# Performance work log

Measured on AMD Instinct MI355X. Metric: run time of the kernel, lower is better.

Reference implementation:

```python
import jax, jax.numpy as jnp
import numpy as np

B, S, D, H = 2, 2048, 1024, 16
HD = D // H  # 64

def setup_inputs() -> dict:
    key = jax.random.key(0)
    ks = jax.random.split(key, 6)
    s = 1.0 / np.sqrt(D)
    return {
        "x": jax.random.normal(ks[0], (B, S, D), dtype=jnp.float32),
        "wq": jax.random.normal(ks[1], (D, D), dtype=jnp.float32) * s,
        "wk": jax.random.normal(ks[2], (D, D), dtype=jnp.float32) * s,
        "wv": jax.random.normal(ks[3], (D, D), dtype=jnp.float32) * s,
        "wo": jax.random.normal(ks[4], (D, D), dtype=jnp.float32) * s,
        "bo": jax.random.normal(ks[5], (D,), dtype=jnp.float32) * 0.01,
    }

def reference(x, wq, wk, wv, wo, bo):
    b, s, _ = x.shape
    # QKV projections (qkvBias=False), reshape to [b, h, s, hd]
    q = (x @ wq).reshape(b, s, H, HD).transpose(0, 2, 1, 3)
    k = (x @ wk).reshape(b, s, H, HD).transpose(0, 2, 1, 3)
    v = (x @ wv).reshape(b, s, H, HD).transpose(0, 2, 1, 3)
    # scores, causal mask (upper triangle -> -inf), scale, softmax
    scores = jnp.einsum('bhqd,bhkd->bhqk', q, k)
    causal = jnp.triu(jnp.ones((s, s), dtype=bool), k=1)
    scores = jnp.where(causal, -jnp.inf, scores) / np.sqrt(HD)
    weights = jax.nn.softmax(scores, axis=-1)  # dropout=0 (eval)
    ctx = jnp.einsum('bhqk,bhkd->bhqd', weights, v)
    ctx = ctx.transpose(0, 2, 1, 3).reshape(b, s, D)
    return ctx @ wo + bo
```

## Files before the change

kernel.cpp:

```cpp
#include <hip/hip_runtime.h>
#include <hip/hip_bf16.h>
#include <math.h>

#define BB 2
#define SS 2048
#define DD 1024
#define HH 16
#define HDIM 64

typedef unsigned short u16;
typedef __attribute__((ext_vector_type(8))) short bfrag;
typedef __attribute__((ext_vector_type(4))) short s16x4;
typedef __attribute__((ext_vector_type(4))) float f32x4;

#define NEG_BIG (-1e30f)
#define QSCALE 0.18033688011112042f

__device__ __forceinline__ u16 f2u(float f) {
    unsigned int u = __builtin_bit_cast(unsigned int, f);
    u += 0x7fffu + ((u >> 16) & 1u);
    return (u16)(u >> 16);
}

__device__ __forceinline__ float fexp2(float x) {
#if __has_builtin(__builtin_amdgcn_exp2f)
    return __builtin_amdgcn_exp2f(x);
#else
    return exp2f(x);
#endif
}

__device__ __forceinline__ void async16(const u16* g, u16* l) {
    __builtin_amdgcn_global_load_lds((__attribute__((address_space(1))) void*)g,
                                     (__attribute__((address_space(3))) void*)l,
                                     16, 0, 0);
}

__device__ __forceinline__ f32x4 mfma16(bfrag a, bfrag b, f32x4 c) {
    return __builtin_amdgcn_mfma_f32_16x16x32_bf16(a, b, c, 0, 0, 0);
}

__device__ __forceinline__ f32x4 mfma_pv(s16x4 a, s16x4 b, f32x4 c) {
#if __has_builtin(__builtin_amdgcn_mfma_f32_16x16x16_bf16)
    return __builtin_amdgcn_mfma_f32_16x16x16_bf16(a, b, c, 0, 0, 0);
#elif __has_builtin(__builtin_amdgcn_mfma_f32_16x16x16bf16_1k)
    return __builtin_amdgcn_mfma_f32_16x16x16bf16_1k(a, b, c, 0, 0, 0);
#else
    f32x4 d;
    asm("v_mfma_f32_16x16x16_bf16 %0, %1, %2, %3" : "=v"(d) : "v"(a), "v"(b), "v"(c));
    return d;
#endif
}

__global__ __launch_bounds__(256) void prep_k(
    const float* __restrict__ x,  u16* __restrict__ xb,
    const float* __restrict__ wq, const float* __restrict__ wk,
    const float* __restrict__ wv, const float* __restrict__ wo,
    u16* __restrict__ wT)
{
    const int id = blockIdx.x;
    const int t = threadIdx.x;
    if (id < 2048) {
        int i = (id * 256 + t) * 8;
        float4 a = *(const float4*)(x + i);
        float4 b = *(const float4*)(x + i + 4);
        u16 o[8] = { f2u(a.x), f2u(a.y), f2u(a.z), f2u(a.w),
                     f2u(b.x), f2u(b.y), f2u(b.z), f2u(b.w) };
        *(uint4*)(xb + i) = *(uint4*)o;
        return;
    }
    const int wid = id - 2048;
    const int z = wid >> 8;
    const int kt = wid & 15, nt = (wid >> 4) & 15;
    const float* w = (z == 0) ? wq : (z == 1) ? wk : (z == 2) ? wv : wo;
    u16* o = wT + (size_t)z * DD * DD;
    __shared__ __align__(16) u16 T[64][72];
    const int k0 = kt * 64, n0 = nt * 64;
    {
        int kr = t >> 2, nb = (t & 3) * 16;
        const float4* s4 = (const float4*)(w + (size_t)(k0 + kr) * DD + n0 + nb);
        #pragma unroll
        for (int jj = 0; jj < 4; ++jj) {
            float4 v = s4[jj];
            T[kr][nb + jj*4 + 0] = f2u(v.x);
            T[kr][nb + jj*4 + 1] = f2u(v.y);
            T[kr][nb + jj*4 + 2] = f2u(v.z);
            T[kr][nb + jj*4 + 3] = f2u(v.w);
        }
    }
    __syncthreads();
    {
        int nr = t >> 2, kb = (t & 3) * 16;
        u16 tmp[16];
        #pragma unroll
        for (int j = 0; j < 16; ++j) tmp[j] = T[kb + j][nr];
        *(uint4*)(o + (size_t)(n0 + nr) * DD + k0 + kb)     = ((uint4*)tmp)[0];
        *(uint4*)(o + (size_t)(n0 + nr) * DD + k0 + kb + 8) = ((uint4*)tmp)[1];
    }
}

__global__ __launch_bounds__(256) void gemm_qkv_k(
    const u16* __restrict__ xb, const u16* __restrict__ wT,
    u16* __restrict__ Qo, u16* __restrict__ Ko, u16* __restrict__ Vt)
{
    const u16* wTz = wT + (size_t)blockIdx.z * DD * DD;
    const float osc = (blockIdx.z == 0) ? QSCALE : 1.0f;

    __shared__ __align__(16) u16 As[128 * 64];
    __shared__ __align__(16) u16 Bs[64 * 64];

    const int t = threadIdx.x;
    const int m0 = blockIdx.x * 128, n0 = blockIdx.y * 64;
    const int lane15 = t & 15, quad = (t >> 4) & 3, wave = t >> 6;
    const int wm = wave & 1, wn = wave >> 1;

    int arow[4], acol[4];
    #pragma unroll
    for (int i = 0; i < 4; ++i) {
        int c = t + i * 256;
        arow[i] = c >> 3;
        acol[i] = (c & 7) ^ (arow[i] & 7);
    }
    const int br0 = t >> 3,         bs0 = t & 7;
    const int br1 = (t + 256) >> 3, bs1 = (t + 256) & 7;
    const int bc0 = bs0 ^ (br0 & 7);
    const int bc1 = bs1 ^ (br1 & 7);
    const int ldb = (t & 192) * 8;

    int aoff[4][2], boff[2][2];
    #pragma unroll
    for (int mi = 0; mi < 4; ++mi) {
        int r = wm * 64 + mi * 16 + lane15;
        #pragma unroll
        for (int kh = 0; kh < 2; ++kh)
            aoff[mi][kh] = (r * 8 + ((kh * 4 + quad) ^ (r & 7))) * 8;
    }
    #pragma unroll
    for (int ni = 0; ni < 2; ++ni) {
        int r = wn * 32 + ni * 16 + lane15;
        #pragma unroll
        for (int kh = 0; kh < 2; ++kh)
            boff[ni][kh] = (r * 8 + ((kh * 4 + quad) ^ (r & 7))) * 8;
    }

    f32x4 acc[4][2];
    #pragma unroll
    for (int mi = 0; mi < 4; ++mi)
        #pragma unroll
        for (int ni = 0; ni < 2; ++ni)
            acc[mi][ni] = (f32x4){0.f, 0.f, 0.f, 0.f};

    for (int it = 0; it < 16; ++it) {
        const int k0 = it * 64;
        #pragma unroll
        for (int i = 0; i < 4; ++i)
            async16(xb + (size_t)(m0 + arow[i]) * DD + k0 + acol[i] * 8,
                    As + ldb + i * 2048);
        async16(wTz + (size_t)(n0 + br0) * DD + k0 + bc0 * 8, Bs + ldb);
        async16(wTz + (size_t)(n0 + br1) * DD + k0 + bc1 * 8, Bs + ldb + 2048);
        __syncthreads();
        #pragma unroll
        for (int kh = 0; kh < 2; ++kh) {
            bfrag av[4], bv[2];
            #pragma unroll
            for (int mi = 0; mi < 4; ++mi) av[mi] = *(const bfrag*)(As + aoff[mi][kh]);
            #pragma unroll
            for (int ni = 0; ni < 2; ++ni) bv[ni] = *(const bfrag*)(Bs + boff[ni][kh]);
            #pragma unroll
            for (int mi = 0; mi < 4; ++mi)
                #pragma unroll
                for (int ni = 0; ni < 2; ++ni)
                    acc[mi][ni] = mfma16(av[mi], bv[ni], acc[mi][ni]);
        }
        __syncthreads();
    }

    const int h = n0 >> 6;
    const int bq = m0 >> 11;
    const int ms = m0 & (SS - 1);

    if (blockIdx.z != 2) {
        u16* out = (blockIdx.z == 0) ? Qo : Ko;
        u16* dst = out + (((size_t)(bq * HH + h)) * SS) * HDIM;
        #pragma unroll
        for (int mi = 0; mi < 4; ++mi) {
            #pragma unroll
            for (int r = 0; r < 4; ++r) {
                int s = ms + wm * 64 + mi * 16 + quad * 4 + r;
                #pragma unroll
                for (int ni = 0; ni < 2; ++ni) {
                    int hd = wn * 32 + ni * 16 + lane15;
                    dst[(size_t)s * HDIM + hd] = f2u(acc[mi][ni][r] * osc);
                }
            }
        }
    } else {
        u16* T = As;
        __syncthreads();
        #pragma unroll
        for (int mi = 0; mi < 4; ++mi)
            #pragma unroll
            for (int r = 0; r < 4; ++r) {
                int ml = wm * 64 + mi * 16 + quad * 4 + r;
                #pragma unroll
                for (int ni = 0; ni < 2; ++ni) {
                    int nl = wn * 32 + ni * 16 + lane15;
                    T[nl * 128 + (ml ^ ((nl & 7) << 4))] = f2u(acc[mi][ni][r]);
                }
            }
        __syncthreads();
        u16* dst = Vt + ((size_t)(bq * HH + h)) * (HDIM * SS);
        #pragma unroll
        for (int i = 0; i < 4; ++i) {
            int c = t + i * 256;
            int row = c >> 4;
            int mb  = (c & 15) * 8;
            uint4 val = *(const uint4*)&T[row * 128 + (mb ^ ((row & 7) << 4))];
            *(uint4*)(dst + (size_t)row * SS + ms + mb) = val;
        }
    }
}

__global__ __launch_bounds__(256) void gemm_out_k(
    const u16* __restrict__ ctxb, const u16* __restrict__ woT,
    const float* __restrict__ bo, float* __restrict__ out)
{
    __shared__ __align__(16) u16 As[2][4096];
    __shared__ __align__(16) u16 Bs[2][4096];

    const int t = threadIdx.x;
    const int m0 = blockIdx.x * 64, n0 = blockIdx.y * 64;
    const int lane15 = t & 15, quad = (t >> 4) & 3, wave = t >> 6;
    const int wm = wave & 1, wn = wave >> 1;

    const int br0 = t >> 3,         bs0 = t & 7;
    const int br1 = (t + 256) >> 3, bs1 = (t + 256) & 7;
    const int bc0 = bs0 ^ (br0 & 7);
    const int bc1 = bs1 ^ (br1 & 7);
    const int ldb = (t & 192) * 8;

    int aoff[2][2], boff[2][2];
    #pragma unroll
    for (int mi = 0; mi < 2; ++mi) {
        int r = wm * 32 + mi * 16 + lane15;
        #pragma unroll
        for (int kh = 0; kh < 2; ++kh)
            aoff[mi][kh] = (r * 8 + ((kh * 4 + quad) ^ (r & 7))) * 8;
    }
    #pragma unroll
    for (int ni = 0; ni < 2; ++ni) {
        int r = wn * 32 + ni * 16 + lane15;
        #pragma unroll
        for (int kh = 0; kh < 2; ++kh)
            boff[ni][kh] = (r * 8 + ((kh * 4 + quad) ^ (r & 7))) * 8;
    }

    f32x4 acc[2][2];
    #pragma unroll
    for (int mi = 0; mi < 2; ++mi)
        #pragma unroll
        for (int ni = 0; ni < 2; ++ni)
            acc[mi][ni] = (f32x4){0.f, 0.f, 0.f, 0.f};

    for (int it = 0; it < 8; ++it) {
        const int k0 = it * 128;
        #pragma unroll
        for (int hh = 0; hh < 2; ++hh) {
            const int kh64 = k0 + hh * 64;
            async16(ctxb + (size_t)(m0 + br0) * DD + kh64 + bc0 * 8, &As[hh][ldb]);
            async16(ctxb + (size_t)(m0 + br1) * DD + kh64 + bc1 * 8, &As[hh][ldb + 2048]);
            async16(woT  + (size_t)(n0 + br0) * DD + kh64 + bc0 * 8, &Bs[hh][ldb]);
            async16(woT  + (size_t)(n0 + br1) * DD + kh64 + bc1 * 8, &Bs[hh][ldb + 2048]);
        }
        __syncthreads();
        #pragma unroll
        for (int hh = 0; hh < 2; ++hh) {
            #pragma unroll
            for (int kh = 0; kh < 2; ++kh) {
                bfrag av[2], bv[2];
                #pragma unroll
                for (int mi = 0; mi < 2; ++mi) av[mi] = *(const bfrag*)&As[hh][aoff[mi][kh]];
                #pragma unroll
                for (int ni = 0; ni < 2; ++ni) bv[ni] = *(const bfrag*)&Bs[hh][boff[ni][kh]];
                #pragma unroll
                for (int mi = 0; mi < 2; ++mi)
                    #pragma unroll
                    for (int ni = 0; ni < 2; ++ni)
                        acc[mi][ni] = mfma16(av[mi], bv[ni], acc[mi][ni]);
            }
        }
        __syncthreads();
    }

    float bias[2];
    #pragma unroll
    for (int ni = 0; ni < 2; ++ni)
        bias[ni] = bo[n0 + wn * 32 + ni * 16 + lane15];

    #pragma unroll
    for (int mi = 0; mi < 2; ++mi) {
        #pragma unroll
        for (int r = 0; r < 4; ++r) {
            int m = m0 + wm * 32 + mi * 16 + quad * 4 + r;
            #pragma unroll
            for (int ni = 0; ni < 2; ++ni) {
                int n = n0 + wn * 32 + ni * 16 + lane15;
                out[(size_t)m * DD + n] = acc[mi][ni][r] + bias[ni];
            }
        }
    }
}

template<bool MASKED>
__device__ __forceinline__ void qkt_pv(
    const u16* __restrict__ Kc, const u16* __restrict__ Vc,
    const bfrag bq[2], const int koff[2], const int voff[8],
    int kv0, int qg, int quad4, f32x4 acc_o[4], f32x4& acc_s, s16x4 ones4)
{
    f32x4 sT[8];
    #pragma unroll
    for (int ni = 0; ni < 8; ++ni) sT[ni] = (f32x4){0.f, 0.f, 0.f, 0.f};

    __builtin_amdgcn_s_setprio(1);
    #pragma unroll
    for (int kh = 0; kh < 2; ++kh)
        #pragma unroll
        for (int ni = 0; ni < 8; ++ni)
            sT[ni] = mfma16(*(const bfrag*)&Kc[koff[kh] + ni * 1024], bq[kh], sT[ni]);
    __builtin_amdgcn_s_setprio(0);

    #pragma unroll
    for (int ni = 0; ni < 8; ++ni) {
        float pv[4];
        #pragma unroll
        for (int r = 0; r < 4; ++r) {
            float v = sT[ni][r];
            if (MASKED) {
                int kvg = kv0 + ni * 16 + quad4 + r;
                if (kvg > qg) v = NEG_BIG;
            }
            pv[r] = fexp2(v);
        }
        unsigned lo = __builtin_amdgcn_perm(
            __builtin_bit_cast(unsigned, pv[1]),
            __builtin_bit_cast(unsigned, pv[0]), 0x07060302u);
        unsigned hi = __builtin_amdgcn_perm(
            __builtin_bit_cast(unsigned, pv[3]),
            __builtin_bit_cast(unsigned, pv[2]), 0x07060302u);
        s16x4 pf = __builtin_bit_cast(s16x4,
            ((unsigned long long)hi << 32) | (unsigned long long)lo);
        __builtin_amdgcn_s_setprio(1);
        acc_s = mfma_pv(ones4, pf, acc_s);
        #pragma unroll
        for (int nd = 0; nd < 4; ++nd)
            acc_o[nd] = mfma_pv(*(const s16x4*)&Vc[voff[ni] + nd * 2048],
                                pf, acc_o[nd]);
        __builtin_amdgcn_s_setprio(0);
    }
}

__global__ __launch_bounds__(512, 4) void attn_k(
    const u16* __restrict__ Q, const u16* __restrict__ K,
    const u16* __restrict__ Vt, u16* __restrict__ ctx)
{
    __shared__ __align__(16) u16 Ks[2][128 * 64];
    __shared__ __align__(16) u16 Vs[2][64 * 128];
    const int t = threadIdx.x;
    const int lane15 = t & 15, quad = (t >> 4) & 3, wave = t >> 6;
    const int bh = blockIdx.x;
    const int yy = (int)blockIdx.y;
    const int y0 = yy & 7;
    const int qt2 = (yy >> 3) ? y0 : 15 - y0;
    const int q0 = qt2 * 128;
    const int b = bh >> 4, h = bh & 15;
    const u16* Qb = Q  + (size_t)bh * SS * HDIM;
    const u16* Kb = K  + (size_t)bh * SS * HDIM;
    const u16* Vb = Vt + (size_t)bh * HDIM * SS;

    const int kr = t >> 3;
    const u16* kga = Kb + (size_t)kr * HDIM + ((t & 7) ^ (kr & 7)) * 8;
    const int vr = t >> 4;
    const u16* vga = Vb + (size_t)vr * SS + ((((t & 7) ^ (vr & 7)) | (t & 8)) * 8);
    const int ldst = (t & 448) * 8;

    const int r7 = lane15 & 7;
    int koff[2];
    #pragma unroll
    for (int kh = 0; kh < 2; ++kh)
        koff[kh] = (lane15 * 8 + ((kh * 4 + quad) ^ r7)) * 8;
    int voff[8];
    #pragma unroll
    for (int ni = 0; ni < 8; ++ni)
        voff[ni] = lane15 * 128 + ((ni * 2 + (quad >> 1)) ^ r7) * 8 + (quad & 1) * 4;

    const int qrow = q0 + wave * 16 + lane15;
    bfrag bq[2];
    bq[0] = *(const bfrag*)(Qb + (size_t)qrow * HDIM + quad * 8);
    bq[1] = *(const bfrag*)(Qb + (size_t)qrow * HDIM + 32 + quad * 8);
    asm volatile("s_waitcnt vmcnt(0)" ::: "memory");

    async16(kga,                 &Ks[0][ldst]);
    async16(kga + 64 * HDIM,     &Ks[0][ldst + 4096]);
    async16(vga,                 &Vs[0][ldst]);
    async16(vga + 32 * SS,       &Vs[0][ldst + 4096]);
    if (qt2 >= 1) {
        async16(kga + 128 * HDIM,      &Ks[1][ldst]);
        async16(kga + 192 * HDIM,      &Ks[1][ldst + 4096]);
        async16(vga + 128,             &Vs[1][ldst]);
        async16(vga + 32 * SS + 128,   &Vs[1][ldst + 4096]);
    }
    const u16* kpa = kga + 2 * 128 * HDIM;
    const u16* vpa = vga + 2 * 128;

    s16x4 ones4;
    #pragma unroll
    for (int i = 0; i < 4; ++i) ones4[i] = (short)0x3f80;

    f32x4 acc_o[4];
    f32x4 acc_s = (f32x4){0.f, 0.f, 0.f, 0.f};
    #pragma unroll
    for (int nd = 0; nd < 4; ++nd) acc_o[nd] = (f32x4){0.f, 0.f, 0.f, 0.f};

    const int qg = qrow;
    const int quad4 = quad * 4;

    for (int kt = 0; kt < qt2; ++kt) {
        asm volatile("s_waitcnt vmcnt(4)" ::: "memory");
        __builtin_amdgcn_s_barrier();
        qkt_pv<false>(Ks[kt & 1], Vs[kt & 1], bq, koff, voff,
                      kt * 128, qg, quad4, acc_o, acc_s, ones4);
        __builtin_amdgcn_s_barrier();
        if (kt + 2 <= qt2) {
            async16(kpa,             &Ks[kt & 1][ldst]);
            async16(kpa + 64 * HDIM, &Ks[kt & 1][ldst + 4096]);
            async16(vpa,             &Vs[kt & 1][ldst]);
            async16(vpa + 32 * SS,   &Vs[kt & 1][ldst + 4096]);
            kpa += 128 * HDIM;
            vpa += 128;
        }
    }
    asm volatile("s_waitcnt vmcnt(0)" ::: "memory");
    __builtin_amdgcn_s_barrier();
    qkt_pv<true>(Ks[qt2 & 1], Vs[qt2 & 1], bq, koff, voff,
                 qt2 * 128, qg, quad4, acc_o, acc_s, ones4);

    const float inv = 1.f / acc_s[0];
    u16* dst = ctx + ((size_t)b * SS + qrow) * DD + h * HDIM + quad4;
    #pragma unroll
    for (int nd = 0; nd < 4; ++nd) {
        uint2 stw;
        stw.x = (unsigned)f2u(acc_o[nd][0] * inv) |
                ((unsigned)f2u(acc_o[nd][1] * inv) << 16);
        stw.y = (unsigned)f2u(acc_o[nd][2] * inv) |
                ((unsigned)f2u(acc_o[nd][3] * inv) << 16);
        *(uint2*)(dst + nd * 16) = stw;
    }
}

extern "C" void kernel_launch(void* const* d_in, const int* in_sizes, int n_in,
                              void* d_out, int out_size, void* d_ws, size_t ws_size,
                              hipStream_t stream) {
    const float* x  = (const float*)d_in[0];
    const float* wq = (const float*)d_in[1];
    const float* wk = (const float*)d_in[2];
    const float* wv = (const float*)d_in[3];
    const float* wo = (const float*)d_in[4];
    const float* bo = (const float*)d_in[5];
    float* out = (float*)d_out;

    char* ws = (char*)d_ws;
    const size_t MB8 = (size_t)8 * 1024 * 1024;
    u16* xb  = (u16*)(ws);
    u16* wT  = (u16*)(ws + MB8);
    u16* Qb  = (u16*)(ws + 2 * MB8);
    u16* Kb  = (u16*)(ws + 3 * MB8);
    u16* Vt  = (u16*)(ws + 4 * MB8);
    u16* ctxb = xb;

    prep_k    <<<3072, 256, 0, stream>>>(x, xb, wq, wk, wv, wo, wT);
    gemm_qkv_k<<<dim3(32, 16, 3), 256, 0, stream>>>(xb, wT, Qb, Kb, Vt);
    attn_k    <<<dim3(32, 16), 512, 0, stream>>>(Qb, Kb, Vt, ctxb);
    gemm_out_k<<<dim3(64, 16), 256, 0, stream>>>(ctxb, wT + (size_t)3 * DD * DD, bo, out);
}
```

Measured before the change: 166.9 us.

## Process two query row groups per wave in attention to reuse K/V fragments

```diff
diff --git a/kernel.cpp b/kernel.cpp
--- a/kernel.cpp
+++ b/kernel.cpp
@@ -312,54 +312,76 @@
 }
 
 template<bool MASKED>
-__device__ __forceinline__ void qkt_pv(
+__device__ __forceinline__ void qkt_pv2(
     const u16* __restrict__ Kc, const u16* __restrict__ Vc,
-    const bfrag bq[2], const int koff[2], const int voff[8],
-    int kv0, int qg, int quad4, f32x4 acc_o[4], f32x4& acc_s, s16x4 ones4)
+    const bfrag bqA[2], const bfrag bqB[2],
+    const int koff[2], const int voff[8],
+    int kv0, int qgA, int qgB, int quad4,
+    f32x4 accA[4], f32x4& asA, f32x4 accB[4], f32x4& asB, s16x4 ones4)
 {
-    f32x4 sT[8];
-    #pragma unroll
-    for (int ni = 0; ni < 8; ++ni) sT[ni] = (f32x4){0.f, 0.f, 0.f, 0.f};
+    f32x4 sA[8], sB[8];
+    #pragma unroll
+    for (int ni = 0; ni < 8; ++ni) {
+        sA[ni] = (f32x4){0.f, 0.f, 0.f, 0.f};
+        sB[ni] = (f32x4){0.f, 0.f, 0.f, 0.f};
+    }
 
     __builtin_amdgcn_s_setprio(1);
     #pragma unroll
     for (int kh = 0; kh < 2; ++kh)
         #pragma unroll
-        for (int ni = 0; ni < 8; ++ni)
-            sT[ni] = mfma16(*(const bfrag*)&Kc[koff[kh] + ni * 1024], bq[kh], sT[ni]);
+        for (int ni = 0; ni < 8; ++ni) {
+            bfrag kf = *(const bfrag*)&Kc[koff[kh] + ni * 1024];
+            sA[ni] = mfma16(kf, bqA[kh], sA[ni]);
+            sB[ni] = mfma16(kf, bqB[kh], sB[ni]);
+        }
     __builtin_amdgcn_s_setprio(0);
 
     #pragma unroll
     for (int ni = 0; ni < 8; ++ni) {
-        float pv[4];
+        float pA[4], pB[4];
         #pragma unroll
         for (int r = 0; r < 4; ++r) {
-            float v = sT[ni][r];
+            float vA = sA[ni][r], vB = sB[ni][r];
             if (MASKED) {
                 int kvg = kv0 + ni * 16 + quad4 + r;
-                if (kvg > qg) v = NEG_BIG;
+                if (kvg > qgA) vA = NEG_BIG;
+                if (kvg > qgB) vB = NEG_BIG;
             }
-            pv[r] = fexp2(v);
-        }
-        unsigned lo = __builtin_amdgcn_perm(
-            __builtin_bit_cast(unsigned, pv[1]),
-            __builtin_bit_cast(unsigned, pv[0]), 0x07060302u);
-        unsigned hi = __builtin_amdgcn_perm(
-            __builtin_bit_cast(unsigned, pv[3]),
-            __builtin_bit_cast(unsigned, pv[2]), 0x07060302u);
-        s16x4 pf = __builtin_bit_cast(s16x4,
-            ((unsigned long long)hi << 32) | (unsigned long long)lo);
+            pA[r] = fexp2(vA);
+            pB[r] = fexp2(vB);
+        }
+        unsigned loA = __builtin_amdgcn_perm(
+            __builtin_bit_cast(unsigned, pA[1]),
+            __builtin_bit_cast(unsigned, pA[0]), 0x07060302u);
+        unsigned hiA = __builtin_amdgcn_perm(
+            __builtin_bit_cast(unsigned, pA[3]),
+            __builtin_bit_cast(unsigned, pA[2]), 0x07060302u);
+        s16x4 pfA = __builtin_bit_cast(s16x4,
+            ((unsigned long long)hiA << 32) | (unsigned long long)loA);
+        unsigned loB = __builtin_amdgcn_perm(
+            __builtin_bit_cast(unsigned, pB[1]),
+            __builtin_bit_cast(unsigned, pB[0]), 0x07060302u);
+        unsigned hiB = __builtin_amdgcn_perm(
+            __builtin_bit_cast(unsigned, pB[3]),
+            __builtin_bit_cast(unsigned, pB[2]), 0x07060302u);
+        s16x4 pfB = __builtin_bit_cast(s16x4,
+            ((unsigned long long)hiB << 32) | (unsigned long long)loB);
+
         __builtin_amdgcn_s_setprio(1);
-        acc_s = mfma_pv(ones4, pf, acc_s);
-        #pragma unroll
-        for (int nd = 0; nd < 4; ++nd)
-            acc_o[nd] = mfma_pv(*(const s16x4*)&Vc[voff[ni] + nd * 2048],
-                                pf, acc_o[nd]);
+        asA = mfma_pv(ones4, pfA, asA);
+        asB = mfma_pv(ones4, pfB, asB);
+        #pragma unroll
+        for (int nd = 0; nd < 4; ++nd) {
+            s16x4 vf = *(const s16x4*)&Vc[voff[ni] + nd * 2048];
+            accA[nd] = mfma_pv(vf, pfA, accA[nd]);
+            accB[nd] = mfma_pv(vf, pfB, accB[nd]);
+        }
         __builtin_amdgcn_s_setprio(0);
     }
 }
 
-__global__ __launch_bounds__(512, 4) void attn_k(
+__global__ __launch_bounds__(256, 2) void attn_k(
     const u16* __restrict__ Q, const u16* __restrict__ K,
     const u16* __restrict__ Vt, u16* __restrict__ ctx)
 {
@@ -377,11 +399,21 @@
     const u16* Kb = K  + (size_t)bh * SS * HDIM;
     const u16* Vb = Vt + (size_t)bh * HDIM * SS;
 
-    const int kr = t >> 3;
-    const u16* kga = Kb + (size_t)kr * HDIM + ((t & 7) ^ (kr & 7)) * 8;
-    const int vr = t >> 4;
-    const u16* vga = Vb + (size_t)vr * SS + ((((t & 7) ^ (vr & 7)) | (t & 8)) * 8);
-    const int ldst = (t & 448) * 8;
+    const int ks = (t & 7) ^ ((t >> 3) & 7);
+    const u16* kga = Kb + (size_t)(t >> 3) * HDIM + ks * 8;
+    const int vs = (((t & 7) ^ ((t >> 4) & 7)) | (t & 8));
+    const u16* vga = Vb + (size_t)(t >> 4) * SS + vs * 8;
+    const int ldst = (t & 192) * 8;
+
+#define STAGE(BUF, KP, VP)                                                   \
+    do {                                                                     \
+        _Pragma("unroll")                                                    \
+        for (int j = 0; j < 4; ++j)                                          \
+            async16((KP) + (size_t)j * 32 * HDIM, &Ks[BUF][ldst + j * 2048]);\
+        _Pragma("unroll")                                                    \
+        for (int j = 0; j < 4; ++j)                                          \
+            async16((VP) + (size_t)j * 16 * SS, &Vs[BUF][ldst + j * 2048]);  \
+    } while (0)
 
     const int r7 = lane15 & 7;
     int koff[2];
@@ -393,22 +425,18 @@
     for (int ni = 0; ni < 8; ++ni)
         voff[ni] = lane15 * 128 + ((ni * 2 + (quad >> 1)) ^ r7) * 8 + (quad & 1) * 4;
 
-    const int qrow = q0 + wave * 16 + lane15;
-    bfrag bq[2];
-    bq[0] = *(const bfrag*)(Qb + (size_t)qrow * HDIM + quad * 8);
-    bq[1] = *(const bfrag*)(Qb + (size_t)qrow * HDIM + 32 + quad * 8);
+    const int qrowA = q0 + wave * 32 + lane15;
+    const int qrowB = qrowA + 16;
+    bfrag bqA[2], bqB[2];
+    bqA[0] = *(const bfrag*)(Qb + (size_t)qrowA * HDIM + quad * 8);
+    bqA[1] = *(const bfrag*)(Qb + (size_t)qrowA * HDIM + 32 + quad * 8);
+    bqB[0] = *(const bfrag*)(Qb + (size_t)qrowB * HDIM + quad * 8);
+    bqB[1] = *(const bfrag*)(Qb + (size_t)qrowB * HDIM + 32 + quad * 8);
     asm volatile("s_waitcnt vmcnt(0)" ::: "memory");
 
-    async16(kga,                 &Ks[0][ldst]);
-    async16(kga + 64 * HDIM,     &Ks[0][ldst + 4096]);
-    async16(vga,                 &Vs[0][ldst]);
-    async16(vga + 32 * SS,       &Vs[0][ldst + 4096]);
-    if (qt2 >= 1) {
-        async16(kga + 128 * HDIM,      &Ks[1][ldst]);
-        async16(kga + 192 * HDIM,      &Ks[1][ldst + 4096]);
-        async16(vga + 128,             &Vs[1][ldst]);
-        async16(vga + 32 * SS + 128,   &Vs[1][ldst + 4096]);
-    }
+    STAGE(0, kga, vga);
+    if (qt2 >= 1)
+        STAGE(1, kga + 128 * HDIM, vga + 128);
     const u16* kpa = kga + 2 * 128 * HDIM;
     const u16* vpa = vga + 2 * 128;
 
@@ -416,44 +444,63 @@
     #pragma unroll
     for (int i = 0; i < 4; ++i) ones4[i] = (short)0x3f80;
 
-    f32x4 acc_o[4];
-    f32x4 acc_s = (f32x4){0.f, 0.f, 0.f, 0.f};
-    #pragma unroll
-    for (int nd = 0; nd < 4; ++nd) acc_o[nd] = (f32x4){0.f, 0.f, 0.f, 0.f};
-
-    const int qg = qrow;
+    f32x4 accA[4], accB[4];
+    f32x4 asA = (f32x4){0.f, 0.f, 0.f, 0.f};
+    f32x4 asB = (f32x4){0.f, 0.f, 0.f, 0.f};
+    #pragma unroll
+    for (int nd = 0; nd < 4; ++nd) {
+        accA[nd] = (f32x4){0.f, 0.f, 0.f, 0.f};
+        accB[nd] = (f32x4){0.f, 0.f, 0.f, 0.f};
+    }
+
     const int quad4 = quad * 4;
 
     for (int kt = 0; kt < qt2; ++kt) {
-        asm volatile("s_waitcnt vmcnt(4)" ::: "memory");
+        asm volatile("s_waitcnt vmcnt(8)" ::: "memory");
         __builtin_amdgcn_s_barrier();
-        qkt_pv<false>(Ks[kt & 1], Vs[kt & 1], bq, koff, voff,
-                      kt * 128, qg, quad4, acc_o, acc_s, ones4);
+        qkt_pv2<false>(Ks[kt & 1], Vs[kt & 1], bqA, bqB, koff, voff,
+                       kt * 128, qrowA, qrowB, quad4,
+                       accA, asA, accB, asB, ones4);
         __builtin_amdgcn_s_barrier();
         if (kt + 2 <= qt2) {
-            async16(kpa,             &Ks[kt & 1][ldst]);
-            async16(kpa + 64 * HDIM, &Ks[kt & 1][ldst + 4096]);
-            async16(vpa,             &Vs[kt & 1][ldst]);
-            async16(vpa + 32 * SS,   &Vs[kt & 1][ldst + 4096]);
+            STAGE(kt & 1, kpa, vpa);
             kpa += 128 * HDIM;
             vpa += 128;
         }
     }
     asm volatile("s_waitcnt vmcnt(0)" ::: "memory");
     __builtin_amdgcn_s_barrier();
-    qkt_pv<true>(Ks[qt2 & 1], Vs[qt2 & 1], bq, koff, voff,
-                 qt2 * 128, qg, quad4, acc_o, acc_s, ones4);
-
-    const float inv = 1.f / acc_s[0];
-    u16* dst = ctx + ((size_t)b * SS + qrow) * DD + h * HDIM + quad4;
-    #pragma unroll
-    for (int nd = 0; nd < 4; ++nd) {
-        uint2 stw;
-        stw.x = (unsigned)f2u(acc_o[nd][0] * inv) |
-                ((unsigned)f2u(acc_o[nd][1] * inv) << 16);
-        stw.y = (unsigned)f2u(acc_o[nd][2] * inv) |
-                ((unsigned)f2u(acc_o[nd][3] * inv) << 16);
-        *(uint2*)(dst + nd * 16) = stw;
+    qkt_pv2<true>(Ks[qt2 & 1], Vs[qt2 & 1], bqA, bqB, koff, voff,
+                  qt2 * 128, qrowA, qrowB, quad4,
+                  accA, asA, accB, asB, ones4);
+
+#undef STAGE
+
+    {
+        const float inv = 1.f / asA[0];
+        u16* dst = ctx + ((size_t)b * SS + qrowA) * DD + h * HDIM + quad4;
+        #pragma unroll
+        for (int nd = 0; nd < 4; ++nd) {
+            uint2 stw;
+            stw.x = (unsigned)f2u(accA[nd][0] * inv) |
+                    ((unsigned)f2u(accA[nd][1] * inv) << 16);
+            stw.y = (unsigned)f2u(accA[nd][2] * inv) |
+                    ((unsigned)f2u(accA[nd][3] * inv) << 16);
+            *(uint2*)(dst + nd * 16) = stw;
+        }
+    }
+    {
+        const float inv = 1.f / asB[0];
+        u16* dst = ctx + ((size_t)b * SS + qrowB) * DD + h * HDIM + quad4;
+        #pragma unroll
+        for (int nd = 0; nd < 4; ++nd) {
+            uint2 stw;
+            stw.x = (unsigned)f2u(accB[nd][0] * inv) |
+                    ((unsigned)f2u(accB[nd][1] * inv) << 16);
+            stw.y = (unsigned)f2u(accB[nd][2] * inv) |
+                    ((unsigned)f2u(accB[nd][3] * inv) << 16);
+            *(uint2*)(dst + nd * 16) = stw;
+        }
     }
 }
 
@@ -479,6 +526,6 @@
 
     prep_k    <<<3072, 256, 0, stream>>>(x, xb, wq, wk, wv, wo, wT);
     gemm_qkv_k<<<dim3(32, 16, 3), 256, 0, stream>>>(xb, wT, Qb, Kb, Vt);
-    attn_k    <<<dim3(32, 16), 512, 0, stream>>>(Qb, Kb, Vt, ctxb);
+    attn_k    <<<dim3(32, 16), 256, 0, stream>>>(Qb, Kb, Vt, ctxb);
     gemm_out_k<<<dim3(64, 16), 256, 0, stream>>>(ctxb, wT + (size_t)3 * DD * DD, bo, out);
 }
```

Result: no change. 169.9 us (+1.8%).
